# Kernel tuning notes

Hardware: AMD Instinct MI355X
Metric: run time of the kernel (lower is better)

Reference implementation:

```python
import jax, jax.numpy as jnp
import numpy as np

N = 50000   # nodes
E = 300000  # directed edges
IN = 512
H = 256
OUT = 256
K = 4096    # K_target; since K < N, pooled node count Kc == K statically


def setup_inputs() -> dict:
    key = jax.random.key(0)
    ks = jax.random.split(key, 8)
    x = jax.random.normal(ks[0], (N, IN), jnp.float32)
    edge_index = jax.random.randint(ks[1], (2, E), 0, N)
    W1 = jax.random.normal(ks[2], (IN, H), jnp.float32) / np.float32(np.sqrt(IN))
    b1 = jnp.zeros((H,), jnp.float32)
    W2 = jax.random.normal(ks[3], (H, OUT), jnp.float32) / np.float32(np.sqrt(H))
    b2 = jnp.zeros((OUT,), jnp.float32)
    w_score = jax.random.normal(ks[4], (H,), jnp.float32) / np.float32(np.sqrt(H))
    W_skip = jax.random.normal(ks[5], (H, OUT), jnp.float32) / np.float32(np.sqrt(H))
    b_skip = jnp.zeros((OUT,), jnp.float32)
    return dict(x=x, edge_index=edge_index, W1=W1, b1=b1, W2=W2, b2=b2,
                w_score=w_score, W_skip=W_skip, b_skip=b_skip)


def _gcn_sparse(x, src, dst, W, b, n):
    # PyG GCNConv(add_self_loops=True, normalize=True): out = D^{-1/2}(A+I)D^{-1/2} x W + b,
    # degrees computed on dst after adding self loops.
    h = x @ W
    loop = jnp.arange(n)
    s = jnp.concatenate([src, loop])
    d = jnp.concatenate([dst, loop])
    deg = jax.ops.segment_sum(jnp.ones_like(d, h.dtype), d, num_segments=n)
    dinv = jnp.where(deg > 0, jax.lax.rsqrt(deg), 0.0)
    coef = (dinv[s] * dinv[d])[:, None]
    return jax.ops.segment_sum(h[s] * coef, d, num_segments=n) + b


def _forward(x, edge_index, W1, b1, W2, b2, w_score, W_skip, b_skip):
    n = x.shape[0]
    src, dst = edge_index[0], edge_index[1]

    # conv1 + relu (dropout is identity in eval mode)
    x1 = jax.nn.relu(_gcn_sparse(x, src, dst, W1, b1, n))
    raw = x1 @ w_score                       # [N] score (Linear, no bias)
    x1g = x1 * jnp.tanh(raw)[:, None]        # gated features

    # top-K node selection
    _, kept = jax.lax.top_k(raw, K)          # sorted descending, like torch.topk
    keep_mask = jnp.zeros((n,), bool).at[kept].set(True)
    deg = jax.ops.segment_sum(jnp.ones((src.shape[0],), jnp.int32), src, num_segments=n)

    # cluster ids: kept nodes get 0..K-1 in topk order
    cid = jnp.full((n,), -1, jnp.int32).at[kept].set(jnp.arange(K, dtype=jnp.int32))

    # non-kept nodes join the kept (undirected) neighbor with max degree;
    # encode (degree, -node_id) so segment_max picks max degree, tie-break smallest id
    s_all = jnp.concatenate([src, dst])
    t_all = jnp.concatenate([dst, src])
    cand = jnp.where(keep_mask[t_all], deg[t_all] * n + (n - 1 - t_all), -1)
    best = jax.ops.segment_max(cand, s_all, num_segments=n)  # empty segs -> int min
    has = best >= 0
    best_t = (n - 1) - jnp.where(has, best % n, 0)
    # global fallback: kept node with max degree (tie-break: earliest in topk order)
    enc_k = deg[kept] * K + (K - 1 - jnp.arange(K))
    bg = kept[jnp.argmax(enc_k)]
    cid = jnp.where(keep_mask, cid, jnp.where(has, cid[best_t], cid[bg]))

    # mean pooling per cluster (pool_by_partition)
    sums = jax.ops.segment_sum(x1g, cid, num_segments=K)
    cnt = jnp.maximum(jax.ops.segment_sum(jnp.ones((n,), x.dtype), cid, num_segments=K), 1.0)
    xp = sums / cnt[:, None]

    # pooled edges with dedup + self-pair removal, as dense KxK adjacency (rows = dst)
    cu, cv = cid[src], cid[dst]
    A = jnp.zeros((K, K), x.dtype).at[cv, cu].max((cu != cv).astype(x.dtype))
    Ahat = A + jnp.eye(K, dtype=x.dtype)
    di = jax.lax.rsqrt(Ahat.sum(axis=1))     # deg >= 1 from self loops
    An = di[:, None] * Ahat * di[None, :]

    # conv2 on pooled graph, broadcast back, skip connection
    xp2 = An @ (xp @ W2) + b2
    return xp2[cid] + x1 @ W_skip + b_skip


def reference(x, edge_index, W1, b1, W2, b2, w_score, W_skip, b_skip):
    return _forward(x, edge_index, W1, b1, W2, b2, w_score, W_skip, b_skip)
```

## Files before the change

### kernel.cpp

```cpp
#include <hip/hip_runtime.h>
#include <hip/hip_bf16.h>

#define N_NODES 50000
#define E_EDGES 300000
#define IN_F 512
#define H_F 256
#define OUT_F 256
#define K_CL 4096
#define KW (K_CL / 32)
#define PCH 128
#define THRESH 192
#define MAXH 1024
#define NSPL 32
#define NB2 ((N_NODES + 255) / 256)

typedef short bh8 __attribute__((ext_vector_type(8)));
typedef float f4 __attribute__((ext_vector_type(4)));
typedef unsigned short u16;

__device__ __forceinline__ unsigned fkey(float f) {
    unsigned u = __float_as_uint(f);
    return (u & 0x80000000u) ? ~u : (u | 0x80000000u);
}

__device__ __forceinline__ u16 f2bf(float f) {
    __hip_bfloat16 b = __float2bfloat16(f);
    return *reinterpret_cast<u16*>(&b);
}

__global__ __launch_bounds__(256) void init_nodes(int* cntD, int* degS,
                                                  unsigned long long* best_enc,
                                                  int* bgnode, int* heavycnt,
                                                  unsigned long long* bestpack) {
    int i = blockIdx.x * blockDim.x + threadIdx.x;
    if (i < N_NODES) { cntD[i] = 0; degS[i] = 0; best_enc[i] = 0ULL; }
    if (i == 0) { *heavycnt = 0; *bgnode = 0x7FFFFFFF; *bestpack = 0ULL; }
}

__global__ __launch_bounds__(256) void deg_edges(const int* __restrict__ src,
                                                 const int* __restrict__ dst,
                                                 int* cntD, int* degS) {
    int e = blockIdx.x * blockDim.x + threadIdx.x;
    if (e >= E_EDGES) return;
    atomicAdd(&cntD[dst[e]], 1);
    atomicAdd(&degS[src[e]], 1);
}

#define SBM 64
#define SBN 128
#define SBK 16
__global__ __launch_bounds__(256) void gemm_f32s(const float* __restrict__ A,
                                                 const float* __restrict__ B,
                                                 float* __restrict__ C,
                                                 int M, int Nc, int Kd) {
    __shared__ float As[2][SBM][SBK];
    __shared__ float Bs[2][SBK][SBN];
    int tid = threadIdx.x;
    int tx = tid & 15;
    int ty = tid >> 4;
    int lane = tid & 63;
    int wave = tid >> 6;
    int row0 = blockIdx.y * SBM, col0 = blockIdx.x * SBN;
    float acc[4][8] = {};

    int arow = wave * 16 + (lane >> 2);
    int acolf = ((((lane & 3) * 16) ^ (((lane >> 4) & 1) << 5)) >> 2);

    auto stage_B = [&](int k0, int bb) {
        #pragma unroll
        for (int u = 0; u < 2; ++u) {
            int chunk = wave * 2 + u;
            int krow = chunk * 2 + (lane >> 5);
            const float* gsrc = &B[(long)(k0 + krow) * Nc + col0 + (lane & 31) * 4];
            __builtin_amdgcn_global_load_lds(
                (const __attribute__((address_space(1))) void*)gsrc,
                (__attribute__((address_space(3))) void*)&Bs[bb][chunk * 2][0],
                16, 0, 0);
        }
    };
    auto stage_A = [&](int k0, int bb) {
        int gr = row0 + arow;
        if (gr > M - 1) gr = M - 1;
        const float* gsrc = &A[(long)gr * Kd + k0 + acolf];
        __builtin_amdgcn_global_load_lds(
            (const __attribute__((address_space(1))) void*)gsrc,
            (__attribute__((address_space(3))) void*)&As[bb][wave * 16][0],
            16, 0, 0);
    };
    auto compute = [&](int bb) {
        #pragma unroll
        for (int kq = 0; kq < 4; ++kq) {
            float4 af[4];
            #pragma unroll
            for (int i = 0; i < 4; ++i) {
                int row = ty * 4 + i;
                int cb = ((kq * 16 ^ (((row >> 2) & 1) << 5)) >> 2);
                af[i] = *(const float4*)&As[bb][row][cb];
            }
            #pragma unroll
            for (int kk = 0; kk < 4; ++kk) {
                int k = kq * 4 + kk;
                float4 b0 = *(const float4*)&Bs[bb][k][tx * 4];
                float4 b1 = *(const float4*)&Bs[bb][k][tx * 4 + 64];
                float bv[8] = {b0.x, b0.y, b0.z, b0.w, b1.x, b1.y, b1.z, b1.w};
                float av[4] = {af[0][kk], af[1][kk], af[2][kk], af[3][kk]};
                #pragma unroll
                for (int i = 0; i < 4; ++i)
                    #pragma unroll
                    for (int j = 0; j < 8; ++j)
                        acc[i][j] += av[i] * bv[j];
            }
        }
    };

    stage_B(0, 0);
    stage_A(0, 0);
    __syncthreads();
    int nt = Kd / SBK;
    for (int t = 0; t < nt; ++t) {
        int cb = t & 1;
        if (t + 1 < nt) {
            stage_B(SBK * (t + 1), cb ^ 1);
            stage_A(SBK * (t + 1), cb ^ 1);
        }
        compute(cb);
        __syncthreads();
    }

    #pragma unroll
    for (int i = 0; i < 4; ++i) {
        int gr = row0 + ty * 4 + i;
        if (gr >= M) continue;
        float4 o0 = {acc[i][0], acc[i][1], acc[i][2], acc[i][3]};
        float4 o1 = {acc[i][4], acc[i][5], acc[i][6], acc[i][7]};
        *(float4*)&C[(long)gr * Nc + col0 + tx * 4] = o0;
        *(float4*)&C[(long)gr * Nc + col0 + 64 + tx * 4] = o1;
    }
}

__global__ __launch_bounds__(256) void pack_W2(const float* __restrict__ Wa, u16* Bpa,
                                               const float* __restrict__ Wb, u16* Bpb) {
    int k = blockIdx.x & 255;
    const float* W = (blockIdx.x < 256) ? Wa : Wb;
    u16* Bp = (blockIdx.x < 256) ? Bpa : Bpb;
    int col = threadIdx.x;
    int kb = k >> 5, g = (k >> 3) & 3, j = k & 7;
    Bp[(((long)(kb * 4 + g) * 256) + col) * 8 + j] = f2bf(W[(long)k * 256 + col]);
}

__global__ __launch_bounds__(256) void gemm_mfma(const u16* __restrict__ Ab,
                                                 const float* __restrict__ Af32,
                                                 const int* __restrict__ cnt,
                                                 const u16* __restrict__ Bp,
                                                 float* __restrict__ C,
                                                 int M,
                                                 const int* __restrict__ cid,
                                                 const float* __restrict__ xp2,
                                                 const float* __restrict__ bskip) {
    int tid = threadIdx.x;
    int w = tid >> 6, l = tid & 63;
    int lo16 = l & 15, hi4 = l >> 4;
    int arow = blockIdx.x * 64 + w * 16 + lo16;
    f4 acc[16];
    #pragma unroll
    for (int n = 0; n < 16; ++n) acc[n] = (f4){0.f, 0.f, 0.f, 0.f};

    float s = 1.f;
    if (Af32 && arow < M) s = 1.f / fmaxf((float)cnt[arow], 1.f);

    #pragma unroll
    for (int kb = 0; kb < 8; ++kb) {
        bh8 a = {0, 0, 0, 0, 0, 0, 0, 0};
        if (arow < M) {
            if (Af32) {
                float4 v0 = *(const float4*)&Af32[(long)arow * 256 + kb * 32 + hi4 * 8];
                float4 v1 = *(const float4*)&Af32[(long)arow * 256 + kb * 32 + hi4 * 8 + 4];
                u16 tmp[8] = {f2bf(v0.x * s), f2bf(v0.y * s), f2bf(v0.z * s), f2bf(v0.w * s),
                              f2bf(v1.x * s), f2bf(v1.y * s), f2bf(v1.z * s), f2bf(v1.w * s)};
                a = *(const bh8*)tmp;
            } else {
                a = *(const bh8*)&Ab[(long)arow * 256 + kb * 32 + hi4 * 8];
            }
        }
        const u16* bbase = &Bp[(((long)(kb * 4 + hi4)) * 256 + lo16) * 8];
        #pragma unroll
        for (int n = 0; n < 16; ++n) {
            bh8 b = *(const bh8*)&bbase[(long)n * 128];
            acc[n] = __builtin_amdgcn_mfma_f32_16x16x32_bf16(a, b, acc[n], 0, 0, 0);
        }
    }

    int orow0 = blockIdx.x * 64 + w * 16 + hi4 * 4;
    #pragma unroll
    for (int r = 0; r < 4; ++r) {
        int gr = orow0 + r;
        if (gr >= M) continue;
        long rb = (long)gr * 256;
        const float* xrow = cid ? (xp2 + (long)cid[gr] * 256) : nullptr;
        #pragma unroll
        for (int n = 0; n < 16; ++n) {
            int gc = n * 16 + lo16;
            float v = acc[n][r];
            if (cid) v += xrow[gc] + bskip[gc];
            C[rb + gc] = v;
        }
    }
}

__global__ __launch_bounds__(256) void scan_l1(const int* __restrict__ cnt,
                                               int* bsum, int n, float* dinv) {
    __shared__ int s[256];
    int t = threadIdx.x;
    int i = blockIdx.x * 256 + t;
    int v = (i < n) ? cnt[i] : 0;
    if (dinv && i < n) dinv[i] = rsqrtf((float)v + 1.0f);
    s[t] = v;
    __syncthreads();
    for (int off = 128; off > 0; off >>= 1) {
        if (t < off) s[t] += s[t + off];
        __syncthreads();
    }
    if (t == 0) bsum[blockIdx.x] = s[0];
}

__global__ __launch_bounds__(256) void scan_l2(const int* __restrict__ bsum,
                                               int* bstart, int nb) {
    __shared__ int s[256];
    int t = threadIdx.x;
    int v = (t < nb) ? bsum[t] : 0;
    s[t] = v;
    __syncthreads();
    for (int off = 1; off < 256; off <<= 1) {
        int a = (t >= off) ? s[t - off] : 0;
        __syncthreads();
        s[t] += a;
        __syncthreads();
    }
    if (t < nb) bstart[t] = s[t] - v;
}

__global__ __launch_bounds__(256) void scan_l3(const int* __restrict__ cnt,
                                               const int* __restrict__ bstart,
                                               int* start, int* cur, int n) {
    __shared__ int s[256];
    int t = threadIdx.x;
    int i = blockIdx.x * 256 + t;
    int v = (i < n) ? cnt[i] : 0;
    s[t] = v;
    __syncthreads();
    for (int off = 1; off < 256; off <<= 1) {
        int a = (t >= off) ? s[t - off] : 0;
        __syncthreads();
        s[t] += a;
        __syncthreads();
    }
    int st = bstart[blockIdx.x] + s[t] - v;
    if (i < n) { start[i] = st; cur[i] = st; }
    if (i == n - 1) start[n] = st + v;
}

__global__ __launch_bounds__(256) void csr_scatter(const int* __restrict__ src,
                                                   const int* __restrict__ dst,
                                                   int* cur, int* csr) {
    int e = blockIdx.x * blockDim.x + threadIdx.x;
    if (e >= E_EDGES) return;
    int d = dst[e];
    int p = atomicAdd(&cur[d], 1);
    csr[p] = src[e];
}

__global__ __launch_bounds__(256) void agg_fused(const float* __restrict__ h,
                                                 const float* __restrict__ dinv,
                                                 const int* __restrict__ rowptr,
                                                 const int* __restrict__ csr,
                                                 const float* __restrict__ b1,
                                                 const float* __restrict__ w_score,
                                                 float* x1, u16* x1b, float* raw) {
    __shared__ int s_src[128];
    __shared__ float s_cf[128];
    __shared__ float red[256];
    int i = blockIdx.x, j = threadIdx.x;
    float di_ = dinv[i];
    float acc = di_ * di_ * h[(long)i * H_F + j];
    int p0 = rowptr[i], p1 = rowptr[i + 1];
    for (int base = p0; base < p1; base += 128) {
        int m = p1 - base; if (m > 128) m = 128;
        if (j < m) { int s = csr[base + j]; s_src[j] = s; s_cf[j] = dinv[s]; }
        __syncthreads();
        #pragma unroll 4
        for (int t = 0; t < m; ++t)
            acc += (s_cf[t] * di_) * h[(long)s_src[t] * H_F + j];
        __syncthreads();
    }
    float v = fmaxf(acc + b1[j], 0.f);
    x1[(long)i * H_F + j] = v;
    x1b[(long)i * H_F + j] = f2bf(v);
    red[j] = v * w_score[j];
    __syncthreads();
    for (int off = 128; off > 0; off >>= 1) {
        if (j < off) red[j] += red[j + off];
        __syncthreads();
    }
    if (j == 0) raw[i] = red[0];
}

__global__ __launch_bounds__(1024) void topk_select(const float* __restrict__ raw,
                                                    unsigned* outT, int* outNeedEq) {
    __shared__ unsigned hist[256];
    __shared__ unsigned sh_prefix;
    __shared__ int sh_k;
    int tid = threadIdx.x;
    if (tid == 0) { sh_prefix = 0; sh_k = K_CL; }
    __syncthreads();
    for (int byte = 3; byte >= 0; --byte) {
        if (tid < 256) hist[tid] = 0;
        __syncthreads();
        unsigned prefix = sh_prefix;
        unsigned known_mask = (byte == 3) ? 0u : (0xFFFFFFFFu << ((byte + 1) * 8));
        for (int i = tid; i < N_NODES; i += 1024) {
            unsigned key = fkey(raw[i]);
            if ((key & known_mask) == prefix)
                atomicAdd(&hist[(key >> (byte * 8)) & 255], 1u);
        }
        __syncthreads();
        if (tid == 0) {
            int kk = sh_k;
            int cum = 0;
            int v = 255;
            for (; v > 0; --v) {
                int c = (int)hist[v];
                if (cum + c >= kk) break;
                cum += c;
            }
            sh_prefix = prefix | ((unsigned)v << (byte * 8));
            sh_k = kk - cum;
        }
        __syncthreads();
    }
    if (tid == 0) { *outT = sh_prefix; *outNeedEq = sh_k; }
}

__global__ __launch_bounds__(256) void topk_count(const float* __restrict__ raw,
                                                  const unsigned* pT,
                                                  int* bGt, int* bEq) {
    __shared__ int sg[256], se[256];
    unsigned T = *pT;
    int t = threadIdx.x;
    int i = blockIdx.x * 256 + t;
    int gt = 0, eq = 0;
    if (i < N_NODES) {
        unsigned k = fkey(raw[i]);
        gt = k > T; eq = (k == T);
    }
    sg[t] = gt; se[t] = eq;
    __syncthreads();
    for (int off = 128; off > 0; off >>= 1) {
        if (t < off) { sg[t] += sg[t + off]; se[t] += se[t + off]; }
        __syncthreads();
    }
    if (t == 0) { bGt[blockIdx.x] = sg[0]; bEq[blockIdx.x] = se[0]; }
}

__global__ __launch_bounds__(256) void scan_blocks(const int* __restrict__ bGt,
                                                   const int* __restrict__ bEq,
                                                   int* gtStart, int* eqStart) {
    __shared__ int sg[256], se[256];
    int t = threadIdx.x;
    int vg = (t < NB2) ? bGt[t] : 0;
    int ve = (t < NB2) ? bEq[t] : 0;
    sg[t] = vg; se[t] = ve;
    __syncthreads();
    for (int off = 1; off < 256; off <<= 1) {
        int a = (t >= off) ? sg[t - off] : 0;
        int b = (t >= off) ? se[t - off] : 0;
        __syncthreads();
        sg[t] += a; se[t] += b;
        __syncthreads();
    }
    if (t < NB2) { gtStart[t] = sg[t] - vg; eqStart[t] = se[t] - ve; }
    if (t == 255) gtStart[NB2] = sg[255];
}

__global__ __launch_bounds__(256) void topk_assign(const float* __restrict__ raw,
                                                   const unsigned* pT, const int* pNeedEq,
                                                   const int* __restrict__ degS,
                                                   const int* __restrict__ gtStart,
                                                   const int* __restrict__ eqStart,
                                                   int* keep, int* cid,
                                                   unsigned long long* bestpack) {
    __shared__ int sg[256], se[256];
    unsigned T = *pT;
    int needEq = *pNeedEq;
    int totalGt = gtStart[NB2];
    int b = blockIdx.x, t = threadIdx.x;
    int i = b * 256 + t;
    int gt = 0, eq = 0;
    unsigned k = 0;
    if (i < N_NODES) {
        k = fkey(raw[i]);
        gt = k > T; eq = (k == T);
    }
    sg[t] = gt; se[t] = eq;
    __syncthreads();
    for (int off = 1; off < 256; off <<= 1) {
        int a = (t >= off) ? sg[t - off] : 0;
        int c = (t >= off) ? se[t - off] : 0;
        __syncthreads();
        sg[t] += a; se[t] += c;
        __syncthreads();
    }
    int eg = sg[t] - gt, ee = se[t] - eq;
    int kp = 0;
    unsigned long long p = 0ULL;
    if (i < N_NODES) {
        int c = -1;
        if (gt) { kp = 1; c = gtStart[b] + eg; }
        else if (eq) {
            int r = eqStart[b] + ee;
            if (r < needEq) { kp = 1; c = totalGt + r; }
        }
        keep[i] = kp; cid[i] = c;
        if (kp) p = ((unsigned long long)(unsigned)degS[i] << 32) | k;
    }
    #pragma unroll
    for (int o = 32; o > 0; o >>= 1) {
        unsigned long long q = __shfl_xor((long long)p, o, 64);
        if (q > p) p = q;
    }
    if ((t & 63) == 0 && p) atomicMax(bestpack, p);
}

__global__ __launch_bounds__(256) void bg_node(const int* __restrict__ keep,
                                               const int* __restrict__ degS,
                                               const float* __restrict__ raw,
                                               const unsigned long long* bestpack, int* bgnode) {
    int i = blockIdx.x * blockDim.x + threadIdx.x;
    if (i < N_NODES && keep[i]) {
        unsigned long long p = ((unsigned long long)(unsigned)degS[i] << 32) | fkey(raw[i]);
        if (p == *bestpack) atomicMin(bgnode, i);
    }
}

__global__ __launch_bounds__(256) void neigh_edges(const int* __restrict__ src,
                                                   const int* __restrict__ dst,
                                                   const int* __restrict__ keep,
                                                   const int* __restrict__ degS,
                                                   unsigned long long* best_enc) {
    int e = blockIdx.x * blockDim.x + threadIdx.x;
    if (e >= 2 * E_EDGES) return;
    int s, t;
    if (e < E_EDGES) { s = src[e]; t = dst[e]; }
    else { s = dst[e - E_EDGES]; t = src[e - E_EDGES]; }
    if (!keep[s] && keep[t]) {
        unsigned long long enc =
            (unsigned long long)((long long)degS[t] * N_NODES + (N_NODES - 1 - t)) + 1ULL;
        atomicMax(&best_enc[s], enc);
    }
}

__global__ __launch_bounds__(256) void resolve_cid(const int* __restrict__ keep,
                                                   const unsigned long long* __restrict__ best_enc,
                                                   const int* __restrict__ bgnode, int* cid) {
    int i = blockIdx.x * blockDim.x + threadIdx.x;
    if (i >= N_NODES) return;
    if (keep[i]) return;
    unsigned long long v = best_enc[i];
    if (v > 0ULL) {
        long long enc = (long long)(v - 1ULL);
        int t = (N_NODES - 1) - (int)(enc % N_NODES);
        cid[i] = cid[t];
    } else {
        cid[i] = cid[*bgnode];
    }
}

#define NPB 1024
__global__ __launch_bounds__(256) void ccount2(const int* __restrict__ cid, int* ccnt) {
    __shared__ int hist[K_CL];
    for (int t = threadIdx.x; t < K_CL; t += 256) hist[t] = 0;
    __syncthreads();
    int base = blockIdx.x * NPB;
    #pragma unroll
    for (int u = 0; u < NPB / 256; ++u) {
        int idx = base + u * 256 + threadIdx.x;
        if (idx < N_NODES) atomicAdd(&hist[cid[idx]], 1);
    }
    __syncthreads();
    for (int t = threadIdx.x; t < K_CL; t += 256) {
        int hh = hist[t];
        if (hh) atomicAdd(&ccnt[t], hh);
    }
}

__global__ __launch_bounds__(256) void cscatter2(const int* __restrict__ cid,
                                                 int* ccur, int* clist) {
    __shared__ int hist[K_CL];
    for (int t = threadIdx.x; t < K_CL; t += 256) hist[t] = 0;
    __syncthreads();
    int base = blockIdx.x * NPB;
    int myc[NPB / 256], myr[NPB / 256];
    #pragma unroll
    for (int u = 0; u < NPB / 256; ++u) {
        int idx = base + u * 256 + threadIdx.x;
        if (idx < N_NODES) { myc[u] = cid[idx]; myr[u] = atomicAdd(&hist[myc[u]], 1); }
        else myc[u] = -1;
    }
    __syncthreads();
    for (int t = threadIdx.x; t < K_CL; t += 256) {
        int hh = hist[t];
        if (hh) hist[t] = atomicAdd(&ccur[t], hh);
    }
    __syncthreads();
    #pragma unroll
    for (int u = 0; u < NPB / 256; ++u)
        if (myc[u] >= 0) clist[hist[myc[u]] + myr[u]] = base + u * 256 + threadIdx.x;
}

__global__ __launch_bounds__(256) void pool_chunk(const float* __restrict__ x1,
                                                  const float* __restrict__ raw,
                                                  const int* __restrict__ clist,
                                                  const int* __restrict__ cid,
                                                  float* xp) {
    __shared__ int s_node[PCH];
    __shared__ int s_c[PCH];
    __shared__ float s_g[PCH];
    int j = threadIdx.x;
    int base = blockIdx.x * PCH;
    int m = N_NODES - base; if (m > PCH) m = PCH;
    for (int t = j; t < m; t += 256) {
        int nd = clist[base + t];
        s_node[t] = nd;
        s_c[t] = cid[nd];
        s_g[t] = tanhf(raw[nd]);
    }
    __syncthreads();
    float acc = 0.f;
    int cprev = s_c[0];
    for (int t = 0; t < m; t += 4) {
        int mm = m - t; if (mm > 4) mm = 4;
        float v[4];
        #pragma unroll
        for (int u = 0; u < 4; ++u)
            if (u < mm) v[u] = x1[(long)s_node[t + u] * H_F + j];
        #pragma unroll
        for (int u = 0; u < 4; ++u) {
            if (u < mm) {
                int c = s_c[t + u];
                if (c != cprev) {
                    atomicAdd(&xp[(long)cprev * H_F + j], acc);
                    acc = 0.f;
                    cprev = c;
                }
                acc += s_g[t + u] * v[u];
            }
        }
    }
    atomicAdd(&xp[(long)cprev * H_F + j], acc);
}

__global__ __launch_bounds__(256) void build_Abits(const int* __restrict__ src,
                                                   const int* __restrict__ dst,
                                                   const int* __restrict__ cid,
                                                   unsigned* Abits) {
    int e = blockIdx.x * blockDim.x + threadIdx.x;
    if (e >= E_EDGES) return;
    int cu = cid[src[e]], cv = cid[dst[e]];
    if (cu != cv) atomicOr(&Abits[(long)cv * KW + (cu >> 5)], 1u << (cu & 31));
}

__global__ __launch_bounds__(256) void pop_di2(const unsigned* __restrict__ Abits, float* di,
                                               int* nnzA, int* heavy, int* heavycnt) {
    int i = blockIdx.x * blockDim.x + threadIdx.x;
    if (i >= K_CL) return;
    int c = 0;
    for (int w = 0; w < KW; ++w) c += __popc(Abits[(long)i * KW + w]);
    di[i] = rsqrtf((float)c + 1.0f);
    nnzA[i] = c;
    if (c > THRESH) {
        int p = atomicAdd(heavycnt, 1);
        if (p < MAXH) heavy[p] = i;
    }
}

__global__ __launch_bounds__(256) void spmm_light(const unsigned* __restrict__ Abits,
                                                  const float* __restrict__ xpW2,
                                                  const float* __restrict__ di,
                                                  const float* __restrict__ b2,
                                                  const int* __restrict__ nnzA,
                                                  float* xp2) {
    __shared__ unsigned s_row[KW];
    __shared__ float s_part[3][256];
    int cv = blockIdx.x;
    if (nnzA[cv] > THRESH) return;
    int tid = threadIdx.x;
    int w = tid >> 6, l = tid & 63;
    if (tid < KW) s_row[tid] = Abits[(long)cv * KW + tid];
    __syncthreads();
    float4 a0 = {0.f, 0.f, 0.f, 0.f}, a1 = {0.f, 0.f, 0.f, 0.f};
    const float4* Y4 = (const float4*)xpW2;
    for (int wi = w * 32; wi < w * 32 + 32; wi += 2) {
        unsigned w0 = s_row[wi], w1 = s_row[wi + 1];
        while (w0 | w1) {
            if (w0) {
                int b = __ffs(w0) - 1; w0 &= w0 - 1;
                int cu = wi * 32 + b;
                float d = di[cu];
                float4 y = Y4[(long)cu * 64 + l];
                a0.x += d * y.x; a0.y += d * y.y; a0.z += d * y.z; a0.w += d * y.w;
            }
            if (w1) {
                int b = __ffs(w1) - 1; w1 &= w1 - 1;
                int cu = (wi + 1) * 32 + b;
                float d = di[cu];
                float4 y = Y4[(long)cu * 64 + l];
                a1.x += d * y.x; a1.y += d * y.y; a1.z += d * y.z; a1.w += d * y.w;
            }
        }
    }
    float4 acc = {a0.x + a1.x, a0.y + a1.y, a0.z + a1.z, a0.w + a1.w};
    if (w > 0) *(float4*)&s_part[w - 1][l * 4] = acc;
    __syncthreads();
    if (w == 0) {
        #pragma unroll
        for (int ww = 0; ww < 3; ++ww) {
            float4 p = *(float4*)&s_part[ww][l * 4];
            acc.x += p.x; acc.y += p.y; acc.z += p.z; acc.w += p.w;
        }
        float dv = di[cv];
        float4 ys = Y4[(long)cv * 64 + l];
        float4 o;
        o.x = dv * (acc.x + dv * ys.x) + b2[l * 4 + 0];
        o.y = dv * (acc.y + dv * ys.y) + b2[l * 4 + 1];
        o.z = dv * (acc.z + dv * ys.z) + b2[l * 4 + 2];
        o.w = dv * (acc.w + dv * ys.w) + b2[l * 4 + 3];
        *(float4*)&xp2[(long)cv * H_F + l * 4] = o;
    }
}

__global__ __launch_bounds__(256) void spmm_heavy(const unsigned* __restrict__ Abits,
                                                  const float* __restrict__ xpW2,
                                                  const float* __restrict__ di,
                                                  const int* __restrict__ heavy,
                                                  const int* __restrict__ heavycnt,
                                                  float* Zacc) {
    __shared__ float s_part[3][256];
    int hi = blockIdx.x;
    int cnt = *heavycnt; if (cnt > MAXH) cnt = MAXH;
    if (hi >= cnt) return;
    int cv = heavy[hi];
    int sp = blockIdx.y;
    int tid = threadIdx.x;
    int w = tid >> 6, l = tid & 63;
    int wi = sp * (KW / NSPL) + w;
    unsigned word = Abits[(long)cv * KW + wi];
    float4 acc = {0.f, 0.f, 0.f, 0.f};
    const float4* Y4 = (const float4*)xpW2;
    while (word) {
        int b = __ffs(word) - 1; word &= word - 1;
        int cu = wi * 32 + b;
        float d = di[cu];
        float4 y = Y4[(long)cu * 64 + l];
        acc.x += d * y.x; acc.y += d * y.y; acc.z += d * y.z; acc.w += d * y.w;
    }
    if (w > 0) *(float4*)&s_part[w - 1][l * 4] = acc;
    __syncthreads();
    if (w == 0) {
        #pragma unroll
        for (int ww = 0; ww < 3; ++ww) {
            float4 p = *(float4*)&s_part[ww][l * 4];
            acc.x += p.x; acc.y += p.y; acc.z += p.z; acc.w += p.w;
        }
        float* zp = &Zacc[(long)cv * H_F + l * 4];
        atomicAdd(zp + 0, acc.x);
        atomicAdd(zp + 1, acc.y);
        atomicAdd(zp + 2, acc.z);
        atomicAdd(zp + 3, acc.w);
    }
}

__global__ __launch_bounds__(256) void heavy_epi(const float* __restrict__ Zacc,
                                                 const float* __restrict__ xpW2,
                                                 const float* __restrict__ di,
                                                 const float* __restrict__ b2,
                                                 const int* __restrict__ heavy,
                                                 const int* __restrict__ heavycnt,
                                                 float* xp2) {
    int hi = blockIdx.x;
    int cnt = *heavycnt; if (cnt > MAXH) cnt = MAXH;
    if (hi >= cnt) return;
    int cv = heavy[hi];
    int j = threadIdx.x;
    float dv = di[cv];
    xp2[(long)cv * H_F + j] =
        dv * (Zacc[(long)cv * H_F + j] + dv * xpW2[(long)cv * H_F + j]) + b2[j];
}

static inline size_t align256(size_t x) { return (x + 255) & ~(size_t)255; }

extern "C" void kernel_launch(void* const* d_in, const int* in_sizes, int n_in,
                              void* d_out, int out_size, void* d_ws, size_t ws_size,
                              hipStream_t stream) {
    const float* x      = (const float*)d_in[0];
    const int*   eidx   = (const int*)d_in[1];
    const float* W1     = (const float*)d_in[2];
    const float* b1     = (const float*)d_in[3];
    const float* W2     = (const float*)d_in[4];
    const float* b2     = (const float*)d_in[5];
    const float* wscore = (const float*)d_in[6];
    const float* Wskip  = (const float*)d_in[7];
    const float* bskip  = (const float*)d_in[8];
    float* out = (float*)d_out;

    const int* src = eidx;
    const int* dst = eidx + E_EDGES;

    char* ws = (char*)d_ws;
    size_t off = 0;
    auto alloc = [&](size_t bytes) { char* p = ws + off; off += align256(bytes); return p; };

    float* h     = (float*)alloc((size_t)N_NODES * H_F * 4);
    float* x1    = (float*)alloc((size_t)N_NODES * H_F * 4);
    u16*   x1b   = (u16*)alloc((size_t)N_NODES * H_F * 2);
    float* raw   = (float*)alloc((size_t)N_NODES * 4);
    float* dinv  = (float*)alloc((size_t)N_NODES * 4);
    int*   cntD  = (int*)alloc((size_t)N_NODES * 4);
    int*   degS  = (int*)alloc((size_t)N_NODES * 4);
    int*   keep  = (int*)alloc((size_t)N_NODES * 4);
    int*   cid   = (int*)alloc((size_t)N_NODES * 4);
    unsigned long long* best_enc = (unsigned long long*)alloc((size_t)N_NODES * 8);
    int*   rowptr= (int*)alloc((size_t)(N_NODES + 1) * 4);
    int*   cur   = (int*)alloc((size_t)N_NODES * 4);
    int*   csr   = (int*)alloc((size_t)E_EDGES * 4);
    int*   ccnt  = (int*)alloc((size_t)K_CL * 4);
    int*   cstart= (int*)alloc((size_t)(K_CL + 1) * 4);
    int*   ccur  = (int*)alloc((size_t)K_CL * 4);
    int*   clist = (int*)alloc((size_t)N_NODES * 4);
    int*   bGt   = (int*)alloc((size_t)NB2 * 4);
    int*   bEq   = (int*)alloc((size_t)NB2 * 4);
    int*   gtStart = (int*)alloc((size_t)(NB2 + 1) * 4);
    int*   eqStart = (int*)alloc((size_t)NB2 * 4);
    int*   bsum  = (int*)alloc((size_t)256 * 4);
    int*   bstart= (int*)alloc((size_t)256 * 4);
    char*  small = alloc(64);
    unsigned* selT = (unsigned*)(small + 0);
    int* needEq    = (int*)(small + 4);
    int* bgnode    = (int*)(small + 8);
    int* heavycnt  = (int*)(small + 12);
    unsigned long long* bestpack = (unsigned long long*)(small + 16);
    float* xp    = (float*)alloc((size_t)K_CL * H_F * 4);
    unsigned* Abits = (unsigned*)alloc((size_t)K_CL * KW * 4);
    float* Zacc  = (float*)alloc((size_t)K_CL * H_F * 4);
    float* di    = (float*)alloc((size_t)K_CL * 4);
    int*   nnzA  = (int*)alloc((size_t)K_CL * 4);
    int*   heavy = (int*)alloc((size_t)MAXH * 4);
    float* xpW2  = (float*)alloc((size_t)K_CL * H_F * 4);
    float* xp2   = (float*)alloc((size_t)K_CL * H_F * 4);
    u16*  BpS   = (u16*)alloc((size_t)H_F * OUT_F * 2);
    u16*  Bp2   = (u16*)alloc((size_t)H_F * H_F * 2);
    (void)ws_size; (void)n_in; (void)in_sizes; (void)out_size;

    int nb = NB2;
    int eb = (E_EDGES + 255) / 256;

    init_nodes<<<nb, 256, 0, stream>>>(cntD, degS, best_enc, bgnode, heavycnt, bestpack);
    deg_edges<<<eb, 256, 0, stream>>>(src, dst, cntD, degS);

    pack_W2<<<512, 256, 0, stream>>>(Wskip, BpS, W2, Bp2);

    {
        dim3 grid(H_F / SBN, (N_NODES + SBM - 1) / SBM);
        gemm_f32s<<<grid, 256, 0, stream>>>(x, W1, h, N_NODES, H_F, IN_F);
    }

    scan_l1<<<NB2, 256, 0, stream>>>(cntD, bsum, N_NODES, dinv);
    scan_l2<<<1, 256, 0, stream>>>(bsum, bstart, NB2);
    scan_l3<<<NB2, 256, 0, stream>>>(cntD, bstart, rowptr, cur, N_NODES);
    csr_scatter<<<eb, 256, 0, stream>>>(src, dst, cur, csr);
    agg_fused<<<N_NODES, 256, 0, stream>>>(h, dinv, rowptr, csr, b1, wscore, x1, x1b, raw);

    topk_select<<<1, 1024, 0, stream>>>(raw, selT, needEq);
    topk_count<<<NB2, 256, 0, stream>>>(raw, selT, bGt, bEq);
    scan_blocks<<<1, 256, 0, stream>>>(bGt, bEq, gtStart, eqStart);
    topk_assign<<<NB2, 256, 0, stream>>>(raw, selT, needEq, degS, gtStart, eqStart,
                                         keep, cid, bestpack);
    bg_node<<<nb, 256, 0, stream>>>(keep, degS, raw, bestpack, bgnode);

    neigh_edges<<<(2 * E_EDGES + 255) / 256, 256, 0, stream>>>(src, dst, keep, degS, best_enc);
    resolve_cid<<<nb, 256, 0, stream>>>(keep, best_enc, bgnode, cid);

    hipMemsetAsync(xp, 0, (size_t)K_CL * H_F * 4 * 2 + (size_t)K_CL * KW * 4, stream);

    hipMemsetAsync(ccnt, 0, (size_t)K_CL * 4, stream);
    {
        int cb = (N_NODES + NPB - 1) / NPB;
        ccount2<<<cb, 256, 0, stream>>>(cid, ccnt);
        scan_l1<<<K_CL / 256, 256, 0, stream>>>(ccnt, bsum, K_CL, nullptr);
        scan_l2<<<1, 256, 0, stream>>>(bsum, bstart, K_CL / 256);
        scan_l3<<<K_CL / 256, 256, 0, stream>>>(ccnt, bstart, cstart, ccur, K_CL);
        cscatter2<<<cb, 256, 0, stream>>>(cid, ccur, clist);
    }
    pool_chunk<<<(N_NODES + PCH - 1) / PCH, 256, 0, stream>>>(x1, raw, clist, cid, xp);

    gemm_mfma<<<K_CL / 64, 256, 0, stream>>>(nullptr, xp, ccnt, Bp2, xpW2, K_CL,
                                             nullptr, nullptr, nullptr);

    build_Abits<<<eb, 256, 0, stream>>>(src, dst, cid, Abits);
    pop_di2<<<(K_CL + 255) / 256, 256, 0, stream>>>(Abits, di, nnzA, heavy, heavycnt);
    spmm_light<<<K_CL, 256, 0, stream>>>(Abits, xpW2, di, b2, nnzA, xp2);
    {
        dim3 hgrid(MAXH, NSPL);
        spmm_heavy<<<hgrid, 256, 0, stream>>>(Abits, xpW2, di, heavy, heavycnt, Zacc);
    }
    heavy_epi<<<MAXH, 256, 0, stream>>>(Zacc, xpW2, di, b2, heavy, heavycnt, xp2);

    gemm_mfma<<<(N_NODES + 63) / 64, 256, 0, stream>>>(x1b, nullptr, nullptr, BpS, out,
                                                       N_NODES, cid, xp2, bskip);
}
```

Measured before the change: 721.3 us.

## Drop fp32 x1 buffer, use single-wave aggregation and bit-packed keep mask

The aggregation kernel now runs one 64-lane wavefront per node, with each lane accumulating four features. This removes the shared-memory staging, block barriers and tree reduction in favour of a shuffle reduction. The fp32 x1 buffer is no longer written; pooling reads the bf16 copy instead, which cuts memory traffic but pools from reduced-precision activations. The per-node keep array is replaced by a ballot-built bitmask to shrink the random reads in the edge and resolve kernels.

```diff
diff --git a/kernel.cpp b/kernel.cpp
--- a/kernel.cpp
+++ b/kernel.cpp
@@ -13,10 +13,12 @@
 #define MAXH 1024
 #define NSPL 32
 #define NB2 ((N_NODES + 255) / 256)
+#define KBW ((N_NODES + 63) / 64 + 8)
 
 typedef short bh8 __attribute__((ext_vector_type(8)));
 typedef float f4 __attribute__((ext_vector_type(4)));
 typedef unsigned short u16;
+typedef unsigned long long u64;
 
 __device__ __forceinline__ unsigned fkey(float f) {
     unsigned u = __float_as_uint(f);
@@ -26,6 +28,14 @@
 __device__ __forceinline__ u16 f2bf(float f) {
     __hip_bfloat16 b = __float2bfloat16(f);
     return *reinterpret_cast<u16*>(&b);
+}
+
+__device__ __forceinline__ float bf2f(u16 u) {
+    return __uint_as_float(((unsigned)u) << 16);
+}
+
+__device__ __forceinline__ int getbit(const u64* __restrict__ bits, int i) {
+    return (int)((bits[i >> 6] >> (i & 63)) & 1ULL);
 }
 
 __global__ __launch_bounds__(256) void init_nodes(int* cntD, int* degS,
@@ -269,39 +279,52 @@
     csr[p] = src[e];
 }
 
-__global__ __launch_bounds__(256) void agg_fused(const float* __restrict__ h,
-                                                 const float* __restrict__ dinv,
-                                                 const int* __restrict__ rowptr,
-                                                 const int* __restrict__ csr,
-                                                 const float* __restrict__ b1,
-                                                 const float* __restrict__ w_score,
-                                                 float* x1, u16* x1b, float* raw) {
-    __shared__ int s_src[128];
-    __shared__ float s_cf[128];
-    __shared__ float red[256];
-    int i = blockIdx.x, j = threadIdx.x;
+__global__ __launch_bounds__(64) void agg_fused(const float* __restrict__ h,
+                                                const float* __restrict__ dinv,
+                                                const int* __restrict__ rowptr,
+                                                const int* __restrict__ csr,
+                                                const float* __restrict__ b1,
+                                                const float* __restrict__ w_score,
+                                                u16* __restrict__ x1b,
+                                                float* __restrict__ raw) {
+    int i = blockIdx.x;
+    int l = threadIdx.x;
     float di_ = dinv[i];
-    float acc = di_ * di_ * h[(long)i * H_F + j];
+    long hb = (long)i * H_F;
+    float sc = di_ * di_;
+    float a0 = sc * h[hb + l];
+    float a1 = sc * h[hb + l + 64];
+    float a2 = sc * h[hb + l + 128];
+    float a3 = sc * h[hb + l + 192];
     int p0 = rowptr[i], p1 = rowptr[i + 1];
-    for (int base = p0; base < p1; base += 128) {
-        int m = p1 - base; if (m > 128) m = 128;
-        if (j < m) { int s = csr[base + j]; s_src[j] = s; s_cf[j] = dinv[s]; }
-        __syncthreads();
-        #pragma unroll 4
-        for (int t = 0; t < m; ++t)
-            acc += (s_cf[t] * di_) * h[(long)s_src[t] * H_F + j];
-        __syncthreads();
-    }
-    float v = fmaxf(acc + b1[j], 0.f);
-    x1[(long)i * H_F + j] = v;
-    x1b[(long)i * H_F + j] = f2bf(v);
-    red[j] = v * w_score[j];
-    __syncthreads();
-    for (int off = 128; off > 0; off >>= 1) {
-        if (j < off) red[j] += red[j + off];
-        __syncthreads();
-    }
-    if (j == 0) raw[i] = red[0];
+    for (int t = p0; t < p1; ++t) {
+        int s = csr[t];
+        float cf = dinv[s] * di_;
+        long sb = (long)s * H_F;
+        a0 += cf * h[sb + l];
+        a1 += cf * h[sb + l + 64];
+        a2 += cf * h[sb + l + 128];
+        a3 += cf * h[sb + l + 192];
+    }
+    float v0 = fmaxf(a0 + b1[l], 0.f);
+    float v1 = fmaxf(a1 + b1[l + 64], 0.f);
+    float v2 = fmaxf(a2 + b1[l + 128], 0.f);
+    float v3 = fmaxf(a3 + b1[l + 192], 0.f);
+    x1b[hb + l] = f2bf(v0);
+    x1b[hb + l + 64] = f2bf(v1);
+    x1b[hb + l + 128] = f2bf(v2);
+    x1b[hb + l + 192] = f2bf(v3);
+    float r0 = v0 * w_score[l];
+    float r1 = v1 * w_score[l + 64];
+    float r2 = v2 * w_score[l + 128];
+    float r3 = v3 * w_score[l + 192];
+    float t1 = r0 + r2;
+    float t2 = r1 + r3;
+    float s2 = t1 + t2;
+    #pragma unroll
+    for (int off = 32; off > 0; off >>= 1)
+        s2 += __shfl_xor(s2, off, 64);
+    if (l == 0) raw[i] = s2;
 }
 
 __global__ __launch_bounds__(1024) void topk_select(const float* __restrict__ raw,
@@ -386,7 +409,7 @@
                                                    const int* __restrict__ degS,
                                                    const int* __restrict__ gtStart,
                                                    const int* __restrict__ eqStart,
-                                                   int* keep, int* cid,
+                                                   u64* keep_bits, int* cid,
                                                    unsigned long long* bestpack) {
     __shared__ int sg[256], se[256];
     unsigned T = *pT;
@@ -419,9 +442,11 @@
             int r = eqStart[b] + ee;
             if (r < needEq) { kp = 1; c = totalGt + r; }
         }
-        keep[i] = kp; cid[i] = c;
+        cid[i] = c;
         if (kp) p = ((unsigned long long)(unsigned)degS[i] << 32) | k;
     }
+    u64 ball = __ballot(kp);
+    if ((t & 63) == 0) keep_bits[(b * 256 + t) >> 6] = ball;
     #pragma unroll
     for (int o = 32; o > 0; o >>= 1) {
         unsigned long long q = __shfl_xor((long long)p, o, 64);
@@ -430,12 +455,12 @@
     if ((t & 63) == 0 && p) atomicMax(bestpack, p);
 }
 
-__global__ __launch_bounds__(256) void bg_node(const int* __restrict__ keep,
+__global__ __launch_bounds__(256) void bg_node(const u64* __restrict__ keep_bits,
                                                const int* __restrict__ degS,
                                                const float* __restrict__ raw,
                                                const unsigned long long* bestpack, int* bgnode) {
     int i = blockIdx.x * blockDim.x + threadIdx.x;
-    if (i < N_NODES && keep[i]) {
+    if (i < N_NODES && getbit(keep_bits, i)) {
         unsigned long long p = ((unsigned long long)(unsigned)degS[i] << 32) | fkey(raw[i]);
         if (p == *bestpack) atomicMin(bgnode, i);
     }
@@ -443,7 +468,7 @@
 
 __global__ __launch_bounds__(256) void neigh_edges(const int* __restrict__ src,
                                                    const int* __restrict__ dst,
-                                                   const int* __restrict__ keep,
+                                                   const u64* __restrict__ keep_bits,
                                                    const int* __restrict__ degS,
                                                    unsigned long long* best_enc) {
     int e = blockIdx.x * blockDim.x + threadIdx.x;
@@ -451,19 +476,19 @@
     int s, t;
     if (e < E_EDGES) { s = src[e]; t = dst[e]; }
     else { s = dst[e - E_EDGES]; t = src[e - E_EDGES]; }
-    if (!keep[s] && keep[t]) {
+    if (!getbit(keep_bits, s) && getbit(keep_bits, t)) {
         unsigned long long enc =
             (unsigned long long)((long long)degS[t] * N_NODES + (N_NODES - 1 - t)) + 1ULL;
         atomicMax(&best_enc[s], enc);
     }
 }
 
-__global__ __launch_bounds__(256) void resolve_cid(const int* __restrict__ keep,
+__global__ __launch_bounds__(256) void resolve_cid(const u64* __restrict__ keep_bits,
                                                    const unsigned long long* __restrict__ best_enc,
                                                    const int* __restrict__ bgnode, int* cid) {
     int i = blockIdx.x * blockDim.x + threadIdx.x;
     if (i >= N_NODES) return;
-    if (keep[i]) return;
+    if (getbit(keep_bits, i)) return;
     unsigned long long v = best_enc[i];
     if (v > 0ULL) {
         long long enc = (long long)(v - 1ULL);
@@ -516,7 +541,7 @@
         if (myc[u] >= 0) clist[hist[myc[u]] + myr[u]] = base + u * 256 + threadIdx.x;
 }
 
-__global__ __launch_bounds__(256) void pool_chunk(const float* __restrict__ x1,
+__global__ __launch_bounds__(256) void pool_chunk(const u16* __restrict__ x1b,
                                                   const float* __restrict__ raw,
                                                   const int* __restrict__ clist,
                                                   const int* __restrict__ cid,
@@ -541,7 +566,7 @@
         float v[4];
         #pragma unroll
         for (int u = 0; u < 4; ++u)
-            if (u < mm) v[u] = x1[(long)s_node[t + u] * H_F + j];
+            if (u < mm) v[u] = bf2f(x1b[(long)s_node[t + u] * H_F + j]);
         #pragma unroll
         for (int u = 0; u < 4; ++u) {
             if (u < mm) {
@@ -719,13 +744,12 @@
     auto alloc = [&](size_t bytes) { char* p = ws + off; off += align256(bytes); return p; };
 
     float* h     = (float*)alloc((size_t)N_NODES * H_F * 4);
-    float* x1    = (float*)alloc((size_t)N_NODES * H_F * 4);
     u16*   x1b   = (u16*)alloc((size_t)N_NODES * H_F * 2);
     float* raw   = (float*)alloc((size_t)N_NODES * 4);
     float* dinv  = (float*)alloc((size_t)N_NODES * 4);
     int*   cntD  = (int*)alloc((size_t)N_NODES * 4);
     int*   degS  = (int*)alloc((size_t)N_NODES * 4);
-    int*   keep  = (int*)alloc((size_t)N_NODES * 4);
+    u64*   keep_bits = (u64*)alloc((size_t)KBW * 8);
     int*   cid   = (int*)alloc((size_t)N_NODES * 4);
     unsigned long long* best_enc = (unsigned long long*)alloc((size_t)N_NODES * 8);
     int*   rowptr= (int*)alloc((size_t)(N_NODES + 1) * 4);
@@ -776,17 +800,18 @@
     scan_l2<<<1, 256, 0, stream>>>(bsum, bstart, NB2);
     scan_l3<<<NB2, 256, 0, stream>>>(cntD, bstart, rowptr, cur, N_NODES);
     csr_scatter<<<eb, 256, 0, stream>>>(src, dst, cur, csr);
-    agg_fused<<<N_NODES, 256, 0, stream>>>(h, dinv, rowptr, csr, b1, wscore, x1, x1b, raw);
+    agg_fused<<<N_NODES, 64, 0, stream>>>(h, dinv, rowptr, csr, b1, wscore, x1b, raw);
 
     topk_select<<<1, 1024, 0, stream>>>(raw, selT, needEq);
     topk_count<<<NB2, 256, 0, stream>>>(raw, selT, bGt, bEq);
     scan_blocks<<<1, 256, 0, stream>>>(bGt, bEq, gtStart, eqStart);
     topk_assign<<<NB2, 256, 0, stream>>>(raw, selT, needEq, degS, gtStart, eqStart,
-                                         keep, cid, bestpack);
-    bg_node<<<nb, 256, 0, stream>>>(keep, degS, raw, bestpack, bgnode);
-
-    neigh_edges<<<(2 * E_EDGES + 255) / 256, 256, 0, stream>>>(src, dst, keep, degS, best_enc);
-    resolve_cid<<<nb, 256, 0, stream>>>(keep, best_enc, bgnode, cid);
+                                         keep_bits, cid, bestpack);
+    bg_node<<<nb, 256, 0, stream>>>(keep_bits, degS, raw, bestpack, bgnode);
+
+    neigh_edges<<<(2 * E_EDGES + 255) / 256, 256, 0, stream>>>(src, dst, keep_bits, degS,
+                                                               best_enc);
+    resolve_cid<<<nb, 256, 0, stream>>>(keep_bits, best_enc, bgnode, cid);
 
     hipMemsetAsync(xp, 0, (size_t)K_CL * H_F * 4 * 2 + (size_t)K_CL * KW * 4, stream);
 
@@ -799,7 +824,7 @@
         scan_l3<<<K_CL / 256, 256, 0, stream>>>(ccnt, bstart, cstart, ccur, K_CL);
         cscatter2<<<cb, 256, 0, stream>>>(cid, ccur, clist);
     }
-    pool_chunk<<<(N_NODES + PCH - 1) / PCH, 256, 0, stream>>>(x1, raw, clist, cid, xp);
+    pool_chunk<<<(N_NODES + PCH - 1) / PCH, 256, 0, stream>>>(x1b, raw, clist, cid, xp);
 
     gemm_mfma<<<K_CL / 64, 256, 0, stream>>>(nullptr, xp, ccnt, Bp2, xpW2, K_CL,
                                              nullptr, nullptr, nullptr);
```

New measurement: 680.6 us. -5.6%, faster.
